# Kernel tuning notes

Hardware: AMD Instinct MI355X
Metric: run time of the kernel (lower is better)

Reference implementation:

```python
import jax, jax.numpy as jnp
import numpy as np
import math

D = 768; H = 12; DH = 64; LAT = 512; B = 2; L = 1024


def _rms(x, w, eps=1e-6):
    return w * x * jax.lax.rsqrt(jnp.mean(x * x, axis=-1, keepdims=True) + eps)


def _rope_tables(seq_len, dh):
    inv = 1.0 / (10000.0 ** (np.arange(0, dh, 2, dtype=np.float32) / dh))
    t = np.arange(seq_len, dtype=np.float32)
    f = np.outer(t, inv)
    emb = np.concatenate([f, f], axis=-1)
    return jnp.asarray(np.cos(emb))[None, :, None, :], jnp.asarray(np.sin(emb))[None, :, None, :]


def _rope(x, cos, sin):
    x1, x2 = jnp.split(x, 2, axis=-1)
    return x * cos + jnp.concatenate([-x2, x1], axis=-1) * sin


def setup_inputs():
    key = jax.random.key(0)
    ks = jax.random.split(key, 8)
    s = 0.02
    return {
        'x': jax.random.normal(ks[0], (B, L, D), jnp.float32),
        'w_ln': jnp.ones((D,), jnp.float32),
        'w_compress': jax.random.normal(ks[1], (D, LAT), jnp.float32) * s,
        'w_qkv': jax.random.normal(ks[2], (LAT, 3 * D), jnp.float32) * s,
        'w_reso': jax.random.normal(ks[3], (LAT, H * 4), jnp.float32) * s,
        'w_qn': jnp.ones((DH,), jnp.float32),
        'w_kn': jnp.ones((DH,), jnp.float32),
        'head_decay': jnp.linspace(-3.0, 1.0, H).astype(jnp.float32),
        'temperature': jnp.ones((1,), jnp.float32) * 0.5,
        'w_out_gate': jax.random.normal(ks[4], (LAT, D), jnp.float32) * s,
        'w_proj': jax.random.normal(ks[5], (D, D), jnp.float32) * s,
        'w_memnorm': jnp.ones((D,), jnp.float32),
    }


def reference(x, w_ln, w_compress, w_qkv, w_reso, w_qn, w_kn, head_decay, temperature, w_out_gate, w_proj, w_memnorm):
    cos, sin = _rope_tables(L, DH)
    xn = _rms(x, w_ln)
    latent = jax.nn.silu(xn @ w_compress)                        # (B,L,LAT)
    q, k, v = jnp.split(latent @ w_qkv, 3, axis=-1)
    q = _rope(_rms(q.reshape(B, L, H, DH), w_qn), cos, sin)
    k = _rope(_rms(k.reshape(B, L, H, DH), w_kn), cos, sin)
    v_f = v.reshape(B, L, H, DH)
    q_f = jax.nn.elu(q) + 1.0
    k_f = jax.nn.elu(k) + 1.0
    params = (latent @ w_reso).reshape(B, L, H, 4)
    sem_amp, sem_phase, ctx_amp, ctx_phase = [params[..., i] for i in range(4)]
    sem_phase = jax.nn.sigmoid(sem_phase) * math.pi
    ctx_phase = jax.nn.sigmoid(ctx_phase) * math.pi
    decay = jnp.clip(0.3 + 0.65 * jax.nn.sigmoid(head_decay), 1e-5, 0.999)   # (H,)
    gate = jnp.clip(jax.nn.sigmoid(jax.nn.sigmoid(sem_amp) * jax.nn.sigmoid(ctx_amp)
                                   * jnp.cos(sem_phase - ctx_phase) * temperature[0]) * 1.2 - 0.1,
                    0.05, 0.95)                                  # (B,L,H)
    one_m = (1.0 - decay)[None, None, :]                          # (1,1,H)
    kv_in = jnp.einsum('blhd,blhe->blhde', k_f, v_f) * gate[..., None, None] * one_m[..., None, None]
    z_in = k_f * one_m[..., None]
    # cumulative log-decay -> df, same as torch cumsum of constant per-step log_decay
    cum_log = jnp.arange(1, L + 1, dtype=jnp.float32)[:, None] * jnp.log(decay)[None, :]
    df = jnp.exp(cum_log)[None, :, :, None]                       # (1,L,H,1)
    kv_states = jnp.cumsum(kv_in / (df[..., None] + 1e-8), axis=1) * df[..., None]
    z_states = jnp.cumsum(z_in / (df + 1e-8), axis=1) * df
    out_num = jnp.einsum('blhd,blhde->blhe', q_f, kv_states)
    den = jnp.clip(jnp.sum(q_f * z_states, axis=-1, keepdims=True), 1e-5, None)
    out = (out_num / den).reshape(B, L, D)
    return (_rms(out, w_memnorm) @ w_proj) * jax.nn.silu(latent @ w_out_gate)
```

## Files before the change

kernel.cpp:

```cpp
#include <hip/hip_runtime.h>
#include <hip/hip_bf16.h>
#include <math.h>

#define D_MODEL 768
#define NHEAD   12
#define LATD    512
#define BATCH   2
#define SEQ     1024
#define NROWS   (BATCH*SEQ)
#define NCHUNK  (SEQ/64)
#define NBH     (BATCH*NHEAD)
#define NFUSE   3200
#define PQ      72

using short8 = __attribute__((ext_vector_type(8))) short;
using f32x4  = __attribute__((ext_vector_type(4))) float;

__device__ __forceinline__ float sigf(float x){ return 1.f/(1.f+expf(-x)); }
__device__ __forceinline__ float decay_of(float hd){
  float d = 0.3f + 0.65f*sigf(hd);
  return fminf(fmaxf(d, 1e-5f), 0.999f);
}
__device__ __forceinline__ unsigned short f2b(float f){
  __hip_bfloat16 h = __float2bfloat16(f);
  return *reinterpret_cast<unsigned short*>(&h);
}
__device__ __forceinline__ float bf2f(unsigned short u){
  unsigned int x = ((unsigned int)u) << 16;
  return __uint_as_float(x);
}
__device__ __forceinline__ void async16(const unsigned short* g, unsigned short* l){
  __builtin_amdgcn_global_load_lds((const __attribute__((address_space(1))) void*)g,
                                   (__attribute__((address_space(3))) void*)l, 16, 0, 0);
}

__device__ __forceinline__ void rms_row(const float* __restrict__ xr,
    const float* __restrict__ w, unsigned short* __restrict__ yr,
    int tid, float* red)
{
  float v0 = xr[tid], v1 = xr[tid+256], v2 = xr[tid+512];
  float s = v0*v0 + v1*v1 + v2*v2;
  #pragma unroll
  for (int off=32; off; off>>=1) s += __shfl_xor(s, off, 64);
  if ((tid & 63) == 0) red[tid>>6] = s;
  __syncthreads();
  s = red[0]+red[1]+red[2]+red[3];
  float sc = rsqrtf(s*(1.f/(float)D_MODEL) + 1e-6f);
  yr[tid]     = f2b(v0*sc*w[tid]);
  yr[tid+256] = f2b(v1*sc*w[tid+256]);
  yr[tid+512] = f2b(v2*sc*w[tid+512]);
}

__global__ __launch_bounds__(256) void k_prep(
    const float* __restrict__ x, const float* __restrict__ w_ln,
    unsigned short* __restrict__ xn,
    const float* __restrict__ wc, const float* __restrict__ wq,
    const float* __restrict__ wr, const float* __restrict__ wg,
    const float* __restrict__ wp, const float* __restrict__ w_mn,
    unsigned short* __restrict__ wtc, unsigned short* __restrict__ wtq,
    unsigned short* __restrict__ wtg, unsigned short* __restrict__ wtp,
    float* __restrict__ sumsq)
{
  __shared__ unsigned short tile[64][65];
  __shared__ float red[4];
  int blk = blockIdx.x, t = threadIdx.x;
  if (blk >= 640){
    int row = blk - 640;
    rms_row(x + (size_t)row*D_MODEL, w_ln, xn + (size_t)row*D_MODEL, t, red);
    return;
  }
  const float* W; unsigned short* WT; int K, N, bx, by;
  const float* kscale = nullptr;
  if (blk < 96){ W=wc; WT=wtc; K=768; N=512; bx=blk&7; by=blk>>3; }
  else if (blk < 384){ int i=blk-96;  W=wq; WT=wtq; K=512; N=2304; bx=i%36; by=i/36; }
  else if (blk < 480){ int i=blk-384; W=wg; WT=wtg; K=512; N=768;  bx=i%12; by=i/12; }
  else if (blk < 624){ int i=blk-480; W=wp; WT=wtp; K=768; N=768;  bx=i%12; by=i/12; kscale=w_mn; }
  else {
    int i = blk - 624;
    if (i == 0){
      #pragma unroll
      for (int j=0;j<8;j++) sumsq[t + j*256] = 0.f;
    }
    #pragma unroll
    for (int j=0;j<16;j++){
      int e = i*4096 + t + j*256;
      int n = 2304 + (e >> 9), k = e & 511;
      float v = (n < 2352) ? wr[(size_t)k*48 + (n-2304)] : 0.f;
      wtq[(size_t)n*512 + k] = f2b(v);
    }
    return;
  }
  int k0 = by*64, n0 = bx*64, cr = t >> 6, cc = t & 63;
  #pragma unroll
  for (int i=0;i<16;i++){
    int r = cr + i*4;
    float v = W[(size_t)(k0+r)*N + n0 + cc];
    if (kscale) v *= kscale[k0+r];
    tile[r][cc] = f2b(v);
  }
  __syncthreads();
  #pragma unroll
  for (int i=0;i<16;i++){
    int nn = cr + i*4;
    WT[(size_t)(n0+nn)*K + k0 + cc] = tile[cc][nn];
  }
}

__global__ __launch_bounds__(256) void k_gemm64(const unsigned short* __restrict__ A,
    const unsigned short* __restrict__ BT, float* __restrict__ Cf,
    unsigned short* __restrict__ Cb, const unsigned short* __restrict__ auxb,
    const float* __restrict__ sums, int M, int N, int K, int act, int NX)
{
  __shared__ unsigned short As[2*64*64];
  __shared__ unsigned short Bs[2*64*64];
  int tid = threadIdx.x;
  int w = tid >> 6, lane = tid & 63;
  int m16 = lane & 15, quad = lane >> 4;
  int bid = blockIdx.x, cpx = gridDim.x >> 3;
  int swz = (bid & 7)*cpx + (bid >> 3);
  int bx = swz % NX, by = swz / NX;
  int bm = by*64, bn = bx*64;

  f32x4 acc[4];
  #pragma unroll
  for (int nt=0;nt<4;nt++) acc[nt] = (f32x4){0.f,0.f,0.f,0.f};

  int nk = K >> 6;
  #pragma unroll
  for (int i=0;i<2;i++){
    int g = (w*2 + i)*64 + lane;
    int m = g >> 3, c = (g & 7) ^ (m & 7);
    async16(A  + (size_t)(bm+m)*K + c*8, As + (w*2+i)*512);
    async16(BT + (size_t)(bn+m)*K + c*8, Bs + (w*2+i)*512);
  }
  __syncthreads();
  int cur = 0;
  for (int t = 0; t < nk; ++t){
    if (t+1 < nk){
      int kk = (t+1) << 6;
      int nb = cur ^ 1;
      #pragma unroll
      for (int i=0;i<2;i++){
        int g = (w*2 + i)*64 + lane;
        int m = g >> 3, c = (g & 7) ^ (m & 7);
        async16(A  + (size_t)(bm+m)*K + kk + c*8, As + nb*4096 + (w*2+i)*512);
        async16(BT + (size_t)(bn+m)*K + kk + c*8, Bs + nb*4096 + (w*2+i)*512);
      }
    }
    #pragma unroll
    for (int s=0;s<2;s++){
      int row = w*16 + m16;
      short8 af = *(const short8*)(As + cur*4096 + (row*8 + ((s*4 + quad) ^ (row & 7)))*8);
      #pragma unroll
      for (int nt=0;nt<4;nt++){
        int n = nt*16 + m16;
        short8 bf = *(const short8*)(Bs + cur*4096 + (n*8 + ((s*4 + quad) ^ (n & 7)))*8);
        acc[nt] = __builtin_amdgcn_mfma_f32_16x16x32_bf16(af, bf, acc[nt], 0, 0, 0);
      }
    }
    __syncthreads();
    cur ^= 1;
  }
  #pragma unroll
  for (int r=0;r<4;r++){
    int row = bm + w*16 + quad*4 + r;
    float rowsc = 1.f;
    if (act == 3) rowsc = rsqrtf(sums[row]*(1.f/(float)D_MODEL) + 1e-6f);
    #pragma unroll
    for (int nt=0;nt<4;nt++){
      int col = bn + nt*16 + m16;
      float v = acc[nt][r];
      if (act == 1) v = v/(1.f + __expf(-v));
      else if (act == 3) v = v*rowsc*bf2f(auxb[(size_t)row*N + col]);
      if (Cf) Cf[(size_t)row*N + col] = v;
      if (Cb) Cb[(size_t)row*N + col] = f2b(v);
    }
  }
}

__global__ __launch_bounds__(256) void k_gemm_fused(const unsigned short* __restrict__ A,
    const unsigned short* __restrict__ BT, const float* __restrict__ w_qn,
    const float* __restrict__ w_kn, const float* __restrict__ hdec,
    const float* __restrict__ temp, unsigned short* __restrict__ qf,
    unsigned short* __restrict__ kf, unsigned short* __restrict__ vf,
    float* __restrict__ cKV, float* __restrict__ cG,
    unsigned short* __restrict__ gateb)
{
  __shared__ __align__(16) unsigned short SM[4*128*64];
  unsigned short* As = SM;
  unsigned short* Bs = SM + 2*128*64;
  const int K = LATD;
  int tid = threadIdx.x;
  int w = tid >> 6, lane = tid & 63;
  int wm = (w >> 1)*64, wn = (w & 1)*64;
  int m16 = lane & 15, quad = lane >> 4;
  int bid = blockIdx.x;
  int swz = (bid & 7)*50 + (bid >> 3);
  int bx = swz >> 4, by = swz & 15;
  int bm = by*128, bn = bx*128;

  f32x4 acc[4][4];
  #pragma unroll
  for (int i=0;i<4;i++)
    #pragma unroll
    for (int j=0;j<4;j++) acc[i][j] = (f32x4){0.f,0.f,0.f,0.f};

  const int nk = K >> 6;
  #pragma unroll
  for (int i=0;i<4;i++){
    int g = (w*4 + i)*64 + lane;
    int m = g >> 3, c = (g & 7) ^ (m & 7);
    async16(A  + (size_t)(bm+m)*K + c*8, As + (w*4+i)*512);
    async16(BT + (size_t)(bn+m)*K + c*8, Bs + (w*4+i)*512);
  }
  __syncthreads();
  int cur = 0;
  for (int t = 0; t < nk; ++t){
    if (t+1 < nk){
      int kk = (t+1) << 6;
      int nb = cur ^ 1;
      #pragma unroll
      for (int i=0;i<4;i++){
        int g = (w*4 + i)*64 + lane;
        int m = g >> 3, c = (g & 7) ^ (m & 7);
        async16(A  + (size_t)(bm+m)*K + kk + c*8, As + nb*8192 + (w*4+i)*512);
        async16(BT + (size_t)(bn+m)*K + kk + c*8, Bs + nb*8192 + (w*4+i)*512);
      }
    }
    #pragma unroll
    for (int s=0;s<2;s++){
      short8 af[4], bf[4];
      #pragma unroll
      for (int mt=0;mt<4;mt++){
        int m = wm + mt*16 + m16;
        int idx = m*8 + ((s*4 + quad) ^ (m & 7));
        af[mt] = *(const short8*)(As + cur*8192 + idx*8);
      }
      #pragma unroll
      for (int nt=0;nt<4;nt++){
        int n = wn + nt*16 + m16;
        int idx = n*8 + ((s*4 + quad) ^ (n & 7));
        bf[nt] = *(const short8*)(Bs + cur*8192 + idx*8);
      }
      #pragma unroll
      for (int mt=0;mt<4;mt++)
        #pragma unroll
        for (int nt=0;nt<4;nt++)
          acc[mt][nt] = __builtin_amdgcn_mfma_f32_16x16x32_bf16(af[mt], bf[nt], acc[mt][nt], 0, 0, 0);
    }
    __syncthreads();
    cur ^= 1;
  }

  int colbase = bn + wn;
  if (colbase < 2304){
    int sec = colbase >= 1536 ? 2 : (colbase >= 768 ? 1 : 0);
    int h = (colbase - sec*768) >> 6;
    if (sec == 2){
      #pragma unroll
      for (int mt=0;mt<4;mt++)
        #pragma unroll
        for (int r=0;r<4;r++){
          int row = bm + wm + mt*16 + quad*4 + r;
          int b = row >> 10, t = row & 1023;
          size_t ob = (((size_t)(b*NHEAD+h))*SEQ + t)*64;
          #pragma unroll
          for (int nt=0;nt<4;nt++)
            vf[ob + nt*16 + m16] = f2b(acc[mt][nt][r]);
        }
    } else {
      const float* wnp = sec ? w_kn : w_qn;
      unsigned short* of = sec ? kf : qf;
      float wv4[4];
      #pragma unroll
      for (int nt=0;nt<4;nt++) wv4[nt] = wnp[nt*16 + m16];
      float inv0 = exp2f(-(float)m16*(1.f/32.f)*13.28771237954945f);
      float inv1 = inv0 * 0.01f;
      #pragma unroll
      for (int mt=0;mt<4;mt++)
        #pragma unroll
        for (int r=0;r<4;r++){
          int row = bm + wm + mt*16 + quad*4 + r;
          int b = row >> 10, t = row & 1023;
          float s = 0.f;
          #pragma unroll
          for (int nt=0;nt<4;nt++) s += acc[mt][nt][r]*acc[mt][nt][r];
          s += __shfl_xor(s, 1, 64); s += __shfl_xor(s, 2, 64);
          s += __shfl_xor(s, 4, 64); s += __shfl_xor(s, 8, 64);
          float rs = rsqrtf(s*(1.f/64.f) + 1e-6f);
          float qv[4];
          #pragma unroll
          for (int nt=0;nt<4;nt++) qv[nt] = acc[mt][nt][r]*rs*wv4[nt];
          float s0,c0,s1,c1;
          __sincosf((float)t*inv0, &s0, &c0);
          __sincosf((float)t*inv1, &s1, &c1);
          size_t ob = (((size_t)(b*NHEAD+h))*SEQ + t)*64;
          #pragma unroll
          for (int nt=0;nt<4;nt++){
            float rot = (nt < 2) ? -qv[nt+2] : qv[nt-2];
            float cs = (nt & 1) ? c1 : c0, sn = (nt & 1) ? s1 : s0;
            float val = qv[nt]*cs + rot*sn;
            val = (val > 0.f) ? val + 1.f : __expf(val);
            of[ob + nt*16 + m16] = f2b(val);
          }
        }
    }
  } else if (colbase < 2432){
    float* pf = (float*)SM;
    if (colbase == 2304){
      #pragma unroll
      for (int mt=0;mt<4;mt++)
        #pragma unroll
        for (int r=0;r<4;r++){
          int rowl = wm + mt*16 + quad*4 + r;
          #pragma unroll
          for (int nt=0;nt<4;nt++){
            int p = nt*16 + m16;
            if (p < 48) pf[rowl*49 + p] = acc[mt][nt][r];
          }
        }
    }
    __syncthreads();
    float tv = temp[0];
    #pragma unroll
    for (int i=0;i<6;i++){
      int idx2 = tid + i*256;
      int rowl = idx2 / 12, h = idx2 - rowl*12;
      int row = bm + rowl, b = row >> 10, t = row & 1023;
      const float* pr = pf + rowl*49 + h*4;
      float sa = sigf(pr[0]);
      float sp = sigf(pr[1])*3.14159265358979323846f;
      float ca = sigf(pr[2]);
      float cp = sigf(pr[3])*3.14159265358979323846f;
      float z = sa*ca*cosf(sp - cp)*tv;
      float gate = fminf(fmaxf(sigf(z)*1.2f - 0.1f, 0.05f), 0.95f);
      float dd = decay_of(hdec[h]);
      float df = expf((float)(t+1)*logf(dd));
      float g = df/(df + 1e-8f);
      int ci = (b*NHEAD + h)*SEQ + t;
      cKV[ci] = g*gate*(1.f - dd);
      cG[ci]  = 1.f/gate;
    }
  } else {
    #pragma unroll
    for (int mt=0;mt<4;mt++)
      #pragma unroll
      for (int r=0;r<4;r++){
        int row = bm + wm + mt*16 + quad*4 + r;
        #pragma unroll
        for (int nt=0;nt<4;nt++){
          int gc = colbase + nt*16 + m16 - 2432;
          float v = acc[mt][nt][r];
          v = v/(1.f + __expf(-v));
          gateb[(size_t)row*D_MODEL + gc] = f2b(v);
        }
      }
  }
}

__global__ __launch_bounds__(256) void k_intra(const unsigned short* __restrict__ qf,
    const unsigned short* __restrict__ kf, const unsigned short* __restrict__ vf,
    const float* __restrict__ cKVb, const float* __restrict__ cGb,
    const float* __restrict__ hdec, float* __restrict__ numb,
    float* __restrict__ denb, float* __restrict__ Pb, float* __restrict__ zPb)
{
  __shared__ __align__(16) unsigned short Qb[64*PQ];
  __shared__ __align__(16) unsigned short Kb[64*PQ];
  __shared__ __align__(16) unsigned short KtS[64*PQ];
  __shared__ __align__(16) unsigned short Wb[64*PQ];
  __shared__ __align__(16) unsigned short Vt[80*PQ];
  __shared__ float cn[64], cps[64];
  int bid = blockIdx.x;
  int chunk = bid & 15, bh = bid >> 4, h = bh % NHEAD;
  int tid = threadIdx.x, w = tid >> 6, lane = tid & 63;
  int m16 = lane & 15, quad = lane >> 4;
  size_t base = ((size_t)bh*SEQ + chunk*64)*64;
  float d = decay_of(hdec[h]);
  float l2d = log2f(d);

  if (tid < 64){
    float c = cKVb[bh*SEQ + chunk*64 + tid];
    float pw = exp2f((float)(63 - tid)*l2d);
    cn[tid] = c;
    cps[tid] = c*pw;
    Vt[64*PQ + tid] = f2b(cGb[bh*SEQ + chunk*64 + tid]);
  }
  for (int i = tid; i < 15*PQ; i += 256) Vt[65*PQ + i] = 0;
  __syncthreads();

  #pragma unroll
  for (int i=0;i<2;i++){
    int g = tid + i*256;
    int r = g >> 3, c8 = (g & 7)*8;
    *(short8*)(Qb + r*PQ + c8) = *(const short8*)(qf + base + r*64 + c8);
    *(short8*)(Kb + r*PQ + c8) = *(const short8*)(kf + base + r*64 + c8);
  }
  {
    int s = tid & 63;
    float cpss = cps[s];
    #pragma unroll
    for (int i=0;i<2;i++){
      int c8 = ((tid >> 6) + i*4)*8;
      short8 vv = *(const short8*)(vf + base + s*64 + c8);
      short8 kk = *(const short8*)(kf + base + s*64 + c8);
      #pragma unroll
      for (int j=0;j<8;j++){
        Vt[(c8+j)*PQ + s] = ((unsigned short*)&vv)[j];
        KtS[(c8+j)*PQ + s] = f2b(bf2f(((unsigned short*)&kk)[j])*cpss);
      }
    }
  }
  __syncthreads();

  int trow = w*16 + quad*4;
  for (int stile=0; stile<4; stile++){
    if (stile > w){
      #pragma unroll
      for (int r=0;r<4;r++) Wb[(trow+r)*PQ + stile*16 + m16] = 0;
      continue;
    }
    f32x4 acc = (f32x4){0.f,0.f,0.f,0.f};
    #pragma unroll
    for (int ks=0;ks<2;ks++){
      short8 a = *(const short8*)(Qb + (w*16 + m16)*PQ + ks*32 + quad*8);
      short8 b = *(const short8*)(Kb + (stile*16 + m16)*PQ + ks*32 + quad*8);
      acc = __builtin_amdgcn_mfma_f32_16x16x32_bf16(a, b, acc, 0, 0, 0);
    }
    int s = stile*16 + m16;
    float cns = cn[s];
    #pragma unroll
    for (int r=0;r<4;r++){
      int t = trow + r;
      float wv = 0.f;
      if (s <= t) wv = acc[r]*exp2f((float)(t-s)*l2d)*cns;
      Wb[t*PQ + s] = f2b(wv);
    }
  }
  __syncthreads();

  {
    f32x4 acc[5];
    #pragma unroll
    for (int et=0;et<5;et++) acc[et] = (f32x4){0.f,0.f,0.f,0.f};
    #pragma unroll
    for (int et=0;et<5;et++)
      #pragma unroll
      for (int ks=0;ks<2;ks++){
        short8 a = *(const short8*)(Wb + (w*16 + m16)*PQ + ks*32 + quad*8);
        short8 b = *(const short8*)(Vt + (et*16 + m16)*PQ + ks*32 + quad*8);
        acc[et] = __builtin_amdgcn_mfma_f32_16x16x32_bf16(a, b, acc[et], 0, 0, 0);
      }
    #pragma unroll
    for (int et=0;et<4;et++)
      #pragma unroll
      for (int r=0;r<4;r++)
        numb[base + (size_t)(trow+r)*64 + et*16 + m16] = acc[et][r];
    if (m16 == 0){
      #pragma unroll
      for (int r=0;r<4;r++)
        denb[bh*SEQ + chunk*64 + trow + r] = acc[4][r];
    }
  }
  {
    #pragma unroll
    for (int j=0;j<5;j++){
      int tIdx = w + 4*j;
      int et = tIdx >> 2, dt = tIdx & 3;
      f32x4 acc = (f32x4){0.f,0.f,0.f,0.f};
      #pragma unroll
      for (int ks=0;ks<2;ks++){
        short8 a = *(const short8*)(Vt  + (et*16 + m16)*PQ + ks*32 + quad*8);
        short8 b = *(const short8*)(KtS + (dt*16 + m16)*PQ + ks*32 + quad*8);
        acc = __builtin_amdgcn_mfma_f32_16x16x32_bf16(a, b, acc, 0, 0, 0);
      }
      if (et < 4){
        #pragma unroll
        for (int r=0;r<4;r++)
          Pb[(size_t)bid*4096 + (et*16 + quad*4 + r)*64 + dt*16 + m16] = acc[r];
      } else {
        if (quad == 0) zPb[bid*64 + dt*16 + m16] = acc[0];
      }
    }
  }
}

__global__ __launch_bounds__(256) void k_cross(const unsigned short* __restrict__ qf,
    const float* __restrict__ Pb, const float* __restrict__ zPb,
    const float* __restrict__ numb, const float* __restrict__ denb,
    const float* __restrict__ hdec, unsigned short* __restrict__ attnb,
    float* __restrict__ sumsq)
{
  __shared__ __align__(16) unsigned short Qb[64*PQ];
  __shared__ __align__(16) unsigned short Sp[80*PQ];
  __shared__ float den_sm[64];
  int bid = blockIdx.x;
  int swz = (bid & 7)*48 + (bid >> 3);
  int chunk = swz & 15, bh = swz >> 4;
  int h = bh % NHEAD, b = bh / NHEAD;
  int tid = threadIdx.x, w = tid >> 6, lane = tid & 63;
  int m16 = lane & 15, quad = lane >> 4;
  size_t base = ((size_t)bh*SEQ + chunk*64)*64;
  float d = decay_of(hdec[h]);
  float l2d = log2f(d);
  float d64l2 = 64.f*l2d;

  #pragma unroll
  for (int i=0;i<2;i++){
    int g = tid + i*256;
    int r = g >> 3, c8 = (g & 7)*8;
    *(short8*)(Qb + r*PQ + c8) = *(const short8*)(qf + base + r*64 + c8);
  }

  {
    int r = tid >> 3, c8 = (tid & 7)*8;
    float a0[8], a1[8];
    #pragma unroll
    for (int j=0;j<8;j++){ a0[j]=0.f; a1[j]=0.f; }
    for (int c=0;c<chunk;c++){
      float wgt = exp2f((float)(chunk-1-c)*d64l2);
      const float* ps = Pb + ((size_t)(bh*NCHUNK + c))*4096;
      float4 p0 = *(const float4*)(ps + r*64 + c8);
      float4 p1 = *(const float4*)(ps + r*64 + c8 + 4);
      float4 p2 = *(const float4*)(ps + (r+32)*64 + c8);
      float4 p3 = *(const float4*)(ps + (r+32)*64 + c8 + 4);
      a0[0]+=wgt*p0.x; a0[1]+=wgt*p0.y; a0[2]+=wgt*p0.z; a0[3]+=wgt*p0.w;
      a0[4]+=wgt*p1.x; a0[5]+=wgt*p1.y; a0[6]+=wgt*p1.z; a0[7]+=wgt*p1.w;
      a1[0]+=wgt*p2.x; a1[1]+=wgt*p2.y; a1[2]+=wgt*p2.z; a1[3]+=wgt*p2.w;
      a1[4]+=wgt*p3.x; a1[5]+=wgt*p3.y; a1[6]+=wgt*p3.z; a1[7]+=wgt*p3.w;
    }
    #pragma unroll
    for (int j=0;j<8;j++){
      Sp[r*PQ + c8 + j]      = f2b(a0[j]);
      Sp[(r+32)*PQ + c8 + j] = f2b(a1[j]);
    }
  }
  if (tid < 64){
    float z = 0.f;
    for (int c=0;c<chunk;c++)
      z += exp2f((float)(chunk-1-c)*d64l2) * zPb[(bh*NCHUNK + c)*64 + tid];
    Sp[64*PQ + tid] = f2b(z);
  }
  for (int i = tid; i < 15*PQ; i += 256) Sp[65*PQ + i] = 0;
  __syncthreads();

  f32x4 acc[5];
  #pragma unroll
  for (int et=0;et<5;et++) acc[et] = (f32x4){0.f,0.f,0.f,0.f};
  #pragma unroll
  for (int et=0;et<5;et++)
    #pragma unroll
    for (int ks=0;ks<2;ks++){
      short8 a = *(const short8*)(Qb + (w*16 + m16)*PQ + ks*32 + quad*8);
      short8 bb = *(const short8*)(Sp + (et*16 + m16)*PQ + ks*32 + quad*8);
      acc[et] = __builtin_amdgcn_mfma_f32_16x16x32_bf16(a, bb, acc[et], 0, 0, 0);
    }
  int trow = w*16 + quad*4;
  if (m16 == 0){
    #pragma unroll
    for (int r=0;r<4;r++){
      int tl = trow + r;
      float pw = exp2f((float)(tl+1)*l2d);
      float den = fmaxf(denb[bh*SEQ + chunk*64 + tl] + pw*acc[4][r], 1e-5f);
      den_sm[tl] = 1.f/den;
    }
  }
  __syncthreads();
  #pragma unroll
  for (int r=0;r<4;r++){
    int tl = trow + r;
    float pw = exp2f((float)(tl+1)*l2d);
    float invden = den_sm[tl];
    int rowg = b*SEQ + chunk*64 + tl;
    float ls = 0.f;
    #pragma unroll
    for (int et=0;et<4;et++){
      int e = et*16 + m16;
      float ov = (numb[base + (size_t)tl*64 + e] + pw*acc[et][r])*invden;
      attnb[(size_t)rowg*D_MODEL + h*64 + e] = f2b(ov);
      ls += ov*ov;
    }
    ls += __shfl_xor(ls, 1, 64); ls += __shfl_xor(ls, 2, 64);
    ls += __shfl_xor(ls, 4, 64); ls += __shfl_xor(ls, 8, 64);
    if (m16 == 0) atomicAdd(&sumsq[rowg], ls);
  }
}

extern "C" void kernel_launch(void* const* d_in, const int* in_sizes, int n_in,
                              void* d_out, int out_size, void* d_ws, size_t ws_size,
                              hipStream_t stream)
{
  (void)in_sizes; (void)n_in; (void)out_size; (void)ws_size;
  const float* x       = (const float*)d_in[0];
  const float* w_ln    = (const float*)d_in[1];
  const float* w_comp  = (const float*)d_in[2];
  const float* w_qkv   = (const float*)d_in[3];
  const float* w_reso  = (const float*)d_in[4];
  const float* w_qn    = (const float*)d_in[5];
  const float* w_kn    = (const float*)d_in[6];
  const float* hdec    = (const float*)d_in[7];
  const float* temp    = (const float*)d_in[8];
  const float* w_ogate = (const float*)d_in[9];
  const float* w_proj  = (const float*)d_in[10];
  const float* w_mn    = (const float*)d_in[11];
  float* ws = (float*)d_ws;
  float* out = (float*)d_out;

  const size_t o_cKV    = 0;
  const size_t o_cG     = o_cKV    + (size_t)NBH*SEQ;
  const size_t o_den    = o_cG     + (size_t)NBH*SEQ;
  const size_t o_P      = o_den    + (size_t)NBH*SEQ;
  const size_t o_zP     = o_P      + (size_t)NBH*NCHUNK*4096;
  const size_t o_sumsq  = o_zP     + (size_t)NBH*NCHUNK*64;
  const size_t o_numb   = o_sumsq  + (size_t)NROWS;
  const size_t o_end    = o_numb   + (size_t)NBH*SEQ*64;

  unsigned short* bws = (unsigned short*)(ws + o_end);
  const size_t u_xn     = 0;
  const size_t u_latent = u_xn     + (size_t)NROWS*D_MODEL;
  const size_t u_memn   = u_latent + (size_t)NROWS*LATD;
  const size_t u_q      = u_memn   + (size_t)NROWS*D_MODEL;
  const size_t u_k      = u_q      + (size_t)NBH*SEQ*64;
  const size_t u_v      = u_k      + (size_t)NBH*SEQ*64;
  const size_t u_gate   = u_v      + (size_t)NBH*SEQ*64;
  const size_t u_wtc    = u_gate   + (size_t)NROWS*D_MODEL;
  const size_t u_wtq    = u_wtc    + (size_t)LATD*D_MODEL;
  const size_t u_wtg    = u_wtq    + (size_t)2432*LATD;
  const size_t u_wtp    = u_wtg    + (size_t)D_MODEL*LATD;

  k_prep<<<2688, 256, 0, stream>>>(x, w_ln, bws + u_xn,
      w_comp, w_qkv, w_reso, w_ogate, w_proj, w_mn,
      bws + u_wtc, bws + u_wtq, bws + u_wtg, bws + u_wtp, ws + o_sumsq);
  k_gemm64<<<256, 256, 0, stream>>>(bws + u_xn, bws + u_wtc,
      nullptr, bws + u_latent, nullptr, nullptr, NROWS, LATD, D_MODEL, 1, LATD/64);
  k_gemm_fused<<<400, 256, 0, stream>>>(bws + u_latent, bws + u_wtq,
      w_qn, w_kn, hdec, temp, bws + u_q, bws + u_k, bws + u_v,
      ws + o_cKV, ws + o_cG, bws + u_gate);
  k_intra<<<NBH*NCHUNK, 256, 0, stream>>>(bws + u_q, bws + u_k, bws + u_v,
      ws + o_cKV, ws + o_cG, hdec, ws + o_numb, ws + o_den, ws + o_P, ws + o_zP);
  k_cross<<<NBH*NCHUNK, 256, 0, stream>>>(bws + u_q, ws + o_P, ws + o_zP,
      ws + o_numb, ws + o_den, hdec, bws + u_memn, ws + o_sumsq);
  k_gemm64<<<384, 256, 0, stream>>>(bws + u_memn, bws + u_wtp,
      out, nullptr, bws + u_gate, ws + o_sumsq, NROWS, D_MODEL, D_MODEL, 3, D_MODEL/64);
}
```

Measured before the change: 150.2 us.

## Fuse intra-chunk and cross-chunk attention kernels with per-head atomic counter barrier

Merges k_intra and k_cross into one k_attn kernel. Intra-chunk numerator and denominator accumulators stay in registers instead of round-tripping through global numb/denb buffers. Chunk states are shared through a per-(batch,head) atomic counter that blocks spin on until all 16 chunks have published their P/zP. This removes one launch and the intermediate global traffic, but relies on all 384 blocks being co-resident to avoid deadlock, and adds spin-wait latency.

```diff
diff --git a/kernel.cpp b/kernel.cpp
--- a/kernel.cpp
+++ b/kernel.cpp
@@ -59,7 +59,7 @@
     const float* __restrict__ wp, const float* __restrict__ w_mn,
     unsigned short* __restrict__ wtc, unsigned short* __restrict__ wtq,
     unsigned short* __restrict__ wtg, unsigned short* __restrict__ wtp,
-    float* __restrict__ sumsq)
+    float* __restrict__ sumsq, int* __restrict__ cnt)
 {
   __shared__ unsigned short tile[64][65];
   __shared__ float red[4];
@@ -80,6 +80,7 @@
     if (i == 0){
       #pragma unroll
       for (int j=0;j<8;j++) sumsq[t + j*256] = 0.f;
+      if (t < 32) cnt[t] = 0;
     }
     #pragma unroll
     for (int j=0;j<16;j++){
@@ -358,25 +359,30 @@
   }
 }
 
-__global__ __launch_bounds__(256) void k_intra(const unsigned short* __restrict__ qf,
+__global__ __launch_bounds__(256) void k_attn(const unsigned short* __restrict__ qf,
     const unsigned short* __restrict__ kf, const unsigned short* __restrict__ vf,
     const float* __restrict__ cKVb, const float* __restrict__ cGb,
-    const float* __restrict__ hdec, float* __restrict__ numb,
-    float* __restrict__ denb, float* __restrict__ Pb, float* __restrict__ zPb)
+    const float* __restrict__ hdec, float* __restrict__ Pb, float* __restrict__ zPb,
+    int* __restrict__ cnt, unsigned short* __restrict__ attnb,
+    float* __restrict__ sumsq)
 {
   __shared__ __align__(16) unsigned short Qb[64*PQ];
   __shared__ __align__(16) unsigned short Kb[64*PQ];
   __shared__ __align__(16) unsigned short KtS[64*PQ];
   __shared__ __align__(16) unsigned short Wb[64*PQ];
   __shared__ __align__(16) unsigned short Vt[80*PQ];
-  __shared__ float cn[64], cps[64];
+  __shared__ float cn[64], cps[64], den_sm[64];
   int bid = blockIdx.x;
-  int chunk = bid & 15, bh = bid >> 4, h = bh % NHEAD;
+  int swz = (bid & 7)*48 + (bid >> 3);
+  int chunk = swz & 15, bh = swz >> 4;
+  int h = bh % NHEAD, b = bh / NHEAD;
   int tid = threadIdx.x, w = tid >> 6, lane = tid & 63;
   int m16 = lane & 15, quad = lane >> 4;
+  int trow = w*16 + quad*4;
   size_t base = ((size_t)bh*SEQ + chunk*64)*64;
   float d = decay_of(hdec[h]);
   float l2d = log2f(d);
+  float d64l2 = 64.f*l2d;
 
   if (tid < 64){
     float c = cKVb[bh*SEQ + chunk*64 + tid];
@@ -412,7 +418,6 @@
   }
   __syncthreads();
 
-  int trow = w*16 + quad*4;
   for (int stile=0; stile<4; stile++){
     if (stile > w){
       #pragma unroll
@@ -423,8 +428,8 @@
     #pragma unroll
     for (int ks=0;ks<2;ks++){
       short8 a = *(const short8*)(Qb + (w*16 + m16)*PQ + ks*32 + quad*8);
-      short8 b = *(const short8*)(Kb + (stile*16 + m16)*PQ + ks*32 + quad*8);
-      acc = __builtin_amdgcn_mfma_f32_16x16x32_bf16(a, b, acc, 0, 0, 0);
+      short8 bb = *(const short8*)(Kb + (stile*16 + m16)*PQ + ks*32 + quad*8);
+      acc = __builtin_amdgcn_mfma_f32_16x16x32_bf16(a, bb, acc, 0, 0, 0);
     }
     int s = stile*16 + m16;
     float cns = cn[s];
@@ -438,29 +443,18 @@
   }
   __syncthreads();
 
-  {
-    f32x4 acc[5];
-    #pragma unroll
-    for (int et=0;et<5;et++) acc[et] = (f32x4){0.f,0.f,0.f,0.f};
-    #pragma unroll
-    for (int et=0;et<5;et++)
-      #pragma unroll
-      for (int ks=0;ks<2;ks++){
-        short8 a = *(const short8*)(Wb + (w*16 + m16)*PQ + ks*32 + quad*8);
-        short8 b = *(const short8*)(Vt + (et*16 + m16)*PQ + ks*32 + quad*8);
-        acc[et] = __builtin_amdgcn_mfma_f32_16x16x32_bf16(a, b, acc[et], 0, 0, 0);
-      }
-    #pragma unroll
-    for (int et=0;et<4;et++)
-      #pragma unroll
-      for (int r=0;r<4;r++)
-        numb[base + (size_t)(trow+r)*64 + et*16 + m16] = acc[et][r];
-    if (m16 == 0){
-      #pragma unroll
-      for (int r=0;r<4;r++)
-        denb[bh*SEQ + chunk*64 + trow + r] = acc[4][r];
-    }
-  }
+  f32x4 accN[5];
+  #pragma unroll
+  for (int et=0;et<5;et++) accN[et] = (f32x4){0.f,0.f,0.f,0.f};
+  #pragma unroll
+  for (int et=0;et<5;et++)
+    #pragma unroll
+    for (int ks=0;ks<2;ks++){
+      short8 a = *(const short8*)(Wb + (w*16 + m16)*PQ + ks*32 + quad*8);
+      short8 bb = *(const short8*)(Vt + (et*16 + m16)*PQ + ks*32 + quad*8);
+      accN[et] = __builtin_amdgcn_mfma_f32_16x16x32_bf16(a, bb, accN[et], 0, 0, 0);
+    }
+
   {
     #pragma unroll
     for (int j=0;j<5;j++){
@@ -470,45 +464,29 @@
       #pragma unroll
       for (int ks=0;ks<2;ks++){
         short8 a = *(const short8*)(Vt  + (et*16 + m16)*PQ + ks*32 + quad*8);
-        short8 b = *(const short8*)(KtS + (dt*16 + m16)*PQ + ks*32 + quad*8);
-        acc = __builtin_amdgcn_mfma_f32_16x16x32_bf16(a, b, acc, 0, 0, 0);
+        short8 bb = *(const short8*)(KtS + (dt*16 + m16)*PQ + ks*32 + quad*8);
+        acc = __builtin_amdgcn_mfma_f32_16x16x32_bf16(a, bb, acc, 0, 0, 0);
       }
       if (et < 4){
         #pragma unroll
         for (int r=0;r<4;r++)
-          Pb[(size_t)bid*4096 + (et*16 + quad*4 + r)*64 + dt*16 + m16] = acc[r];
+          Pb[((size_t)(bh*NCHUNK + chunk))*4096 + (et*16 + quad*4 + r)*64 + dt*16 + m16] = acc[r];
       } else {
-        if (quad == 0) zPb[bid*64 + dt*16 + m16] = acc[0];
-      }
-    }
-  }
-}
-
-__global__ __launch_bounds__(256) void k_cross(const unsigned short* __restrict__ qf,
-    const float* __restrict__ Pb, const float* __restrict__ zPb,
-    const float* __restrict__ numb, const float* __restrict__ denb,
-    const float* __restrict__ hdec, unsigned short* __restrict__ attnb,
-    float* __restrict__ sumsq)
-{
-  __shared__ __align__(16) unsigned short Qb[64*PQ];
-  __shared__ __align__(16) unsigned short Sp[80*PQ];
-  __shared__ float den_sm[64];
-  int bid = blockIdx.x;
-  int swz = (bid & 7)*48 + (bid >> 3);
-  int chunk = swz & 15, bh = swz >> 4;
-  int h = bh % NHEAD, b = bh / NHEAD;
-  int tid = threadIdx.x, w = tid >> 6, lane = tid & 63;
-  int m16 = lane & 15, quad = lane >> 4;
-  size_t base = ((size_t)bh*SEQ + chunk*64)*64;
-  float d = decay_of(hdec[h]);
-  float l2d = log2f(d);
-  float d64l2 = 64.f*l2d;
-
-  #pragma unroll
-  for (int i=0;i<2;i++){
-    int g = tid + i*256;
-    int r = g >> 3, c8 = (g & 7)*8;
-    *(short8*)(Qb + r*PQ + c8) = *(const short8*)(qf + base + r*64 + c8);
+        if (quad == 0) zPb[(bh*NCHUNK + chunk)*64 + dt*16 + m16] = acc[0];
+      }
+    }
+  }
+
+  __syncthreads();
+  __threadfence();
+  if (tid == 0) atomicAdd(&cnt[bh], 1);
+  if (chunk > 0){
+    if (tid == 0){
+      while (__hip_atomic_load(&cnt[bh], __ATOMIC_RELAXED, __HIP_MEMORY_SCOPE_AGENT) < NCHUNK)
+        __builtin_amdgcn_s_sleep(2);
+    }
+    __syncthreads();
+    __threadfence();
   }
 
   {
@@ -530,37 +508,35 @@
     }
     #pragma unroll
     for (int j=0;j<8;j++){
-      Sp[r*PQ + c8 + j]      = f2b(a0[j]);
-      Sp[(r+32)*PQ + c8 + j] = f2b(a1[j]);
+      Vt[r*PQ + c8 + j]      = f2b(a0[j]);
+      Vt[(r+32)*PQ + c8 + j] = f2b(a1[j]);
     }
   }
   if (tid < 64){
     float z = 0.f;
     for (int c=0;c<chunk;c++)
       z += exp2f((float)(chunk-1-c)*d64l2) * zPb[(bh*NCHUNK + c)*64 + tid];
-    Sp[64*PQ + tid] = f2b(z);
-  }
-  for (int i = tid; i < 15*PQ; i += 256) Sp[65*PQ + i] = 0;
-  __syncthreads();
-
-  f32x4 acc[5];
-  #pragma unroll
-  for (int et=0;et<5;et++) acc[et] = (f32x4){0.f,0.f,0.f,0.f};
+    Vt[64*PQ + tid] = f2b(z);
+  }
+  __syncthreads();
+
+  f32x4 acc2[5];
+  #pragma unroll
+  for (int et=0;et<5;et++) acc2[et] = (f32x4){0.f,0.f,0.f,0.f};
   #pragma unroll
   for (int et=0;et<5;et++)
     #pragma unroll
     for (int ks=0;ks<2;ks++){
       short8 a = *(const short8*)(Qb + (w*16 + m16)*PQ + ks*32 + quad*8);
-      short8 bb = *(const short8*)(Sp + (et*16 + m16)*PQ + ks*32 + quad*8);
-      acc[et] = __builtin_amdgcn_mfma_f32_16x16x32_bf16(a, bb, acc[et], 0, 0, 0);
-    }
-  int trow = w*16 + quad*4;
+      short8 bb = *(const short8*)(Vt + (et*16 + m16)*PQ + ks*32 + quad*8);
+      acc2[et] = __builtin_amdgcn_mfma_f32_16x16x32_bf16(a, bb, acc2[et], 0, 0, 0);
+    }
   if (m16 == 0){
     #pragma unroll
     for (int r=0;r<4;r++){
       int tl = trow + r;
       float pw = exp2f((float)(tl+1)*l2d);
-      float den = fmaxf(denb[bh*SEQ + chunk*64 + tl] + pw*acc[4][r], 1e-5f);
+      float den = fmaxf(accN[4][r] + pw*acc2[4][r], 1e-5f);
       den_sm[tl] = 1.f/den;
     }
   }
@@ -575,7 +551,7 @@
     #pragma unroll
     for (int et=0;et<4;et++){
       int e = et*16 + m16;
-      float ov = (numb[base + (size_t)tl*64 + e] + pw*acc[et][r])*invden;
+      float ov = (accN[et][r] + pw*acc2[et][r])*invden;
       attnb[(size_t)rowg*D_MODEL + h*64 + e] = f2b(ov);
       ls += ov*ov;
     }
@@ -607,12 +583,11 @@
 
   const size_t o_cKV    = 0;
   const size_t o_cG     = o_cKV    + (size_t)NBH*SEQ;
-  const size_t o_den    = o_cG     + (size_t)NBH*SEQ;
-  const size_t o_P      = o_den    + (size_t)NBH*SEQ;
+  const size_t o_P      = o_cG     + (size_t)NBH*SEQ;
   const size_t o_zP     = o_P      + (size_t)NBH*NCHUNK*4096;
   const size_t o_sumsq  = o_zP     + (size_t)NBH*NCHUNK*64;
-  const size_t o_numb   = o_sumsq  + (size_t)NROWS;
-  const size_t o_end    = o_numb   + (size_t)NBH*SEQ*64;
+  const size_t o_cnt    = o_sumsq  + (size_t)NROWS;
+  const size_t o_end    = o_cnt    + 32;
 
   unsigned short* bws = (unsigned short*)(ws + o_end);
   const size_t u_xn     = 0;
@@ -629,16 +604,16 @@
 
   k_prep<<<2688, 256, 0, stream>>>(x, w_ln, bws + u_xn,
       w_comp, w_qkv, w_reso, w_ogate, w_proj, w_mn,
-      bws + u_wtc, bws + u_wtq, bws + u_wtg, bws + u_wtp, ws + o_sumsq);
+      bws + u_wtc, bws + u_wtq, bws + u_wtg, bws + u_wtp,
+      ws + o_sumsq, (int*)(ws + o_cnt));
   k_gemm64<<<256, 256, 0, stream>>>(bws + u_xn, bws + u_wtc,
       nullptr, bws + u_latent, nullptr, nullptr, NROWS, LATD, D_MODEL, 1, LATD/64);
   k_gemm_fused<<<400, 256, 0, stream>>>(bws + u_latent, bws + u_wtq,
       w_qn, w_kn, hdec, temp, bws + u_q, bws + u_k, bws + u_v,
       ws + o_cKV, ws + o_cG, bws + u_gate);
-  k_intra<<<NBH*NCHUNK, 256, 0, stream>>>(bws + u_q, bws + u_k, bws + u_v,
-      ws + o_cKV, ws + o_cG, hdec, ws + o_numb, ws + o_den, ws + o_P, ws + o_zP);
-  k_cross<<<NBH*NCHUNK, 256, 0, stream>>>(bws + u_q, ws + o_P, ws + o_zP,
-      ws + o_numb, ws + o_den, hdec, bws + u_memn, ws + o_sumsq);
+  k_attn<<<NBH*NCHUNK, 256, 0, stream>>>(bws + u_q, bws + u_k, bws + u_v,
+      ws + o_cKV, ws + o_cG, hdec, ws + o_P, ws + o_zP,
+      (int*)(ws + o_cnt), bws + u_memn, ws + o_sumsq);
   k_gemm64<<<384, 256, 0, stream>>>(bws + u_memn, bws + u_wtp,
       out, nullptr, bws + u_gate, ws + o_sumsq, NROWS, D_MODEL, D_MODEL, 3, D_MODEL/64);
 }
```

Result: slower. 226.1 us (+50.6%).
